# Kernel tuning notes

Measured on AMD Instinct MI355X. Metric: run time of the kernel, lower is better.

Reference implementation:

```python
import jax, jax.numpy as jnp
import numpy as np

BASIS_PRIMES = (2, 3, 5, 7, 11, 13, 17, 19, 23, 29)


def _build_resonance(max_seq):
    # p-adic valuations v_p(n) for n = 1..max_seq, each basis prime (vectorized LUT build)
    n = np.arange(1, max_seq + 1, dtype=np.int64)
    vals = np.zeros((max_seq, len(BASIS_PRIMES)), dtype=np.float32)
    for j, p in enumerate(BASIS_PRIMES):
        m = n.copy()
        while True:
            div = (m % p) == 0
            if not div.any():
                break
            vals[div, j] += 1.0
            m = np.where(div, m // p, m)
    # resonance(a,b) = sum_i min(v_{p_i}(a), v_{p_i}(b))  -> [T, T]
    res = np.zeros((max_seq, max_seq), dtype=np.float32)
    for j in range(len(BASIS_PRIMES)):
        vj = vals[:, j]
        res += np.minimum(vj[:, None], vj[None, :])
    causal = np.tril(np.ones((max_seq, max_seq), dtype=bool))
    allowed = ((res > 0) | np.eye(max_seq, dtype=bool)) & causal
    bias = (np.log1p(res) * allowed).astype(np.float32)
    return bias, allowed


def setup_inputs() -> dict:
    B, T, d_model, head_size, max_seq = 8, 2048, 1024, 128, 2048
    key = jax.random.key(0)
    kx, kq, kk, kv = jax.random.split(key, 4)
    bound = 1.0 / np.sqrt(d_model)  # torch Linear default init range
    x = jax.random.normal(kx, (B, T, d_model), dtype=jnp.float32)
    Wq = jax.random.uniform(kq, (head_size, d_model), jnp.float32, -bound, bound)
    Wk = jax.random.uniform(kk, (head_size, d_model), jnp.float32, -bound, bound)
    Wv = jax.random.uniform(kv, (head_size, d_model), jnp.float32, -bound, bound)
    bias, allowed = _build_resonance(max_seq)
    return {
        "x": x, "Wq": Wq, "Wk": Wk, "Wv": Wv,
        "resonance_bias": jnp.asarray(bias),
        "allowed": jnp.asarray(allowed),
    }


def reference(x, Wq, Wk, Wv, resonance_bias, allowed):
    B, T, C = x.shape
    q = jnp.einsum('btc,hc->bth', x, Wq)
    k = jnp.einsum('btc,hc->bth', x, Wk)
    v = jnp.einsum('btc,hc->bth', x, Wv)
    # NOTE: original scales by C**-0.5 where C = d_model (input channels)
    wei = jnp.einsum('bth,bsh->bts', q, k) * (C ** -0.5)
    wei = wei + resonance_bias[:T, :T]
    neg = jnp.finfo(wei.dtype).min
    wei = jnp.where(allowed[:T, :T], wei, neg)
    wei = jax.nn.softmax(wei, axis=-1)  # dropout is identity in eval mode
    return jnp.einsum('bts,bsh->bth', wei, v)
```

## Files before the change

### kernel.cpp

```cpp
#include <hip/hip_runtime.h>
#include <hip/hip_bf16.h>
#include <stdint.h>

typedef float f32x4  __attribute__((ext_vector_type(4)));
typedef short s16x8  __attribute__((ext_vector_type(8)));
typedef short s16x4  __attribute__((ext_vector_type(4)));
typedef unsigned short u16x8 __attribute__((ext_vector_type(8)));

#define MFMA16(A,B,C) __builtin_amdgcn_mfma_f32_16x16x32_bf16((A),(B),(C),0,0,0)

__device__ __forceinline__ short f2bf(float f) {
    uint32_t u = __float_as_uint(f);
    u += 0x7FFFu + ((u >> 16) & 1u);
    return (short)(u >> 16);
}
__device__ __forceinline__ float bf2f(unsigned short u) {
    return __uint_as_float(((uint32_t)u) << 16);
}
__device__ __forceinline__ int cum_jobs(int qt) {
  int h = qt >> 1;
  return (qt & 1) ? (h + 1) * (h + 1) : h * (h + 1);
}

#define OFF_PB   0u
#define OFF_WPK  8388608u
#define OFF_PQ   9175040u
#define OFF_PK   13369344u
#define OFF_PV   17563648u
#define OFF_PML  21757952u
#define OFF_PO   22863872u
#define WS_SPLIT 60096512u

__global__ __launch_bounds__(256) void pack_misc_kernel(
    const float* __restrict__ wq, const float* __restrict__ wk,
    const float* __restrict__ wv, const float* __restrict__ bias,
    short* __restrict__ Wpk, short* __restrict__ pb) {
  const int tid = threadIdx.x, wid = tid >> 6, lane = tid & 63;
  const int g = lane >> 4, c4 = lane & 15;
  if (blockIdx.x < 192) {
    const int idx = blockIdx.x * 4 + wid;
    const int im = idx >> 8, rest = idx & 255;
    const int ntl = rest >> 5, k32 = rest & 31;
    const float* w = (im == 0) ? wq : (im == 1) ? wk : wv;
    const float* p = w + (size_t)(ntl * 16 + c4) * 1024 + k32 * 32 + 4 * g;
    f32x4 lo = *(const f32x4*)p;
    f32x4 hi = *(const f32x4*)(p + 16);
    s16x8 o = { f2bf(lo[0]), f2bf(lo[1]), f2bf(lo[2]), f2bf(lo[3]),
                f2bf(hi[0]), f2bf(hi[1]), f2bf(hi[2]), f2bf(hi[3]) };
    *(s16x8*)(Wpk + (size_t)idx * 512 + lane * 8) = o;
  } else {
    const int idx = (blockIdx.x - 192) * 4 + wid;
    const int t16 = idx >> 6, s32 = idx & 63;
    const int t = t16 * 16 + c4;
    const int sb = s32 * 32 + 4 * g;
    const float* p = bias + (size_t)t * 2048 + sb;
    f32x4 lo = *(const f32x4*)p;
    f32x4 hi = *(const f32x4*)(p + 16);
    s16x8 o;
    #pragma unroll
    for (int i = 0; i < 4; ++i) {
      int s0 = sb + i, s1 = sb + 16 + i;
      bool ok0 = (s0 <= t) && (s0 == t || lo[i] > 0.f);
      bool ok1 = (s1 <= t) && (s1 == t || hi[i] > 0.f);
      o[i]     = f2bf(ok0 ? lo[i] : -1e30f);
      o[4 + i] = f2bf(ok1 ? hi[i] : -1e30f);
    }
    *(s16x8*)(pb + (size_t)idx * 512 + lane * 8) = o;
  }
}

__global__ __launch_bounds__(256, 2) void qkv_gemm7_kernel(
    const float* __restrict__ x, const short* __restrict__ Wpk,
    short* __restrict__ pq, short* __restrict__ pk, short* __restrict__ pv) {
  const int tid = threadIdx.x, wid = tid >> 6, lane = tid & 63;
  const int g = lane >> 4, c4 = lane & 15;
  const int L8 = lane * 8;
  const int w = blockIdx.x * 4 + wid;
  const int im = w >> 9;
  const int t2 = w & 511;
  const int b = t2 >> 6;
  const float* xrA = x + (size_t)(t2 * 32 + c4) * 1024 + 4 * g;
  const float* xrB = xrA + (size_t)16 * 1024;
  const short* wp = Wpk + (size_t)(im * 256) * 512 + L8;

  f32x4 acc0[8], acc1[8];
  #pragma unroll
  for (int i = 0; i < 8; ++i) {
    acc0[i] = (f32x4){0.f, 0.f, 0.f, 0.f};
    acc1[i] = (f32x4){0.f, 0.f, 0.f, 0.f};
  }

  f32x4 aA0l, aA0h, aA1l, aA1h;
  f32x4 aB0l, aB0h, aB1l, aB1h;
  s16x8 wA[8], wB[8];
#define G7_LDRAW(p0l, p0h, p1l, p1h, kk) { \
    p0l = *(const f32x4*)(xrA + (size_t)(kk) * 32); \
    p0h = *(const f32x4*)(xrA + (size_t)(kk) * 32 + 16); \
    p1l = *(const f32x4*)(xrB + (size_t)(kk) * 32); \
    p1h = *(const f32x4*)(xrB + (size_t)(kk) * 32 + 16); }
#define G7_LDW(dw, kk) { _Pragma("unroll") \
    for (int nt = 0; nt < 8; ++nt) \
      dw[nt] = *(const s16x8*)(wp + (size_t)(nt * 32 + (kk)) * 512); }
#define G7_CVT(fr, lo, hi) \
    s16x8 fr = { f2bf(lo[0]), f2bf(lo[1]), f2bf(lo[2]), f2bf(lo[3]), \
                 f2bf(hi[0]), f2bf(hi[1]), f2bf(hi[2]), f2bf(hi[3]) };

  if (im < 2) {
    G7_LDRAW(aA0l, aA0h, aA1l, aA1h, 0); G7_LDW(wA, 0);
    for (int k = 0; k < 32; k += 2) {
      G7_LDRAW(aB0l, aB0h, aB1l, aB1h, k + 1); G7_LDW(wB, k + 1);
      G7_CVT(xf0, aA0l, aA0h); G7_CVT(xf1, aA1l, aA1h);
      #pragma unroll
      for (int nt = 0; nt < 8; ++nt) {
        acc0[nt] = MFMA16(wA[nt], xf0, acc0[nt]);
        acc1[nt] = MFMA16(wA[nt], xf1, acc1[nt]);
      }
      if (k + 2 < 32) { G7_LDRAW(aA0l, aA0h, aA1l, aA1h, k + 2); G7_LDW(wA, k + 2); }
      G7_CVT(yf0, aB0l, aB0h); G7_CVT(yf1, aB1l, aB1h);
      #pragma unroll
      for (int nt = 0; nt < 8; ++nt) {
        acc0[nt] = MFMA16(wB[nt], yf0, acc0[nt]);
        acc1[nt] = MFMA16(wB[nt], yf1, acc1[nt]);
      }
    }
    short* __restrict__ o = im ? pk : pq;
    const int loc0 = (t2 & 63) * 2;
    #pragma unroll
    for (int f = 0; f < 4; ++f) {
      s16x8 fr0 = { f2bf(acc0[2*f][0]),   f2bf(acc0[2*f][1]),
                    f2bf(acc0[2*f][2]),   f2bf(acc0[2*f][3]),
                    f2bf(acc0[2*f+1][0]), f2bf(acc0[2*f+1][1]),
                    f2bf(acc0[2*f+1][2]), f2bf(acc0[2*f+1][3]) };
      *(s16x8*)(o + (size_t)(b * 512 + loc0 * 4 + f) * 512 + L8) = fr0;
      s16x8 fr1 = { f2bf(acc1[2*f][0]),   f2bf(acc1[2*f][1]),
                    f2bf(acc1[2*f][2]),   f2bf(acc1[2*f][3]),
                    f2bf(acc1[2*f+1][0]), f2bf(acc1[2*f+1][1]),
                    f2bf(acc1[2*f+1][2]), f2bf(acc1[2*f+1][3]) };
      *(s16x8*)(o + (size_t)(b * 512 + (loc0 + 1) * 4 + f) * 512 + L8) = fr1;
    }
  } else {
    G7_LDRAW(aA0l, aA0h, aA1l, aA1h, 0); G7_LDW(wA, 0);
    for (int k = 0; k < 32; k += 2) {
      G7_LDRAW(aB0l, aB0h, aB1l, aB1h, k + 1); G7_LDW(wB, k + 1);
      G7_CVT(xf0, aA0l, aA0h); G7_CVT(xf1, aA1l, aA1h);
      #pragma unroll
      for (int nt = 0; nt < 8; ++nt) {
        acc0[nt] = MFMA16(xf0, wA[nt], acc0[nt]);
        acc1[nt] = MFMA16(xf1, wA[nt], acc1[nt]);
      }
      if (k + 2 < 32) { G7_LDRAW(aA0l, aA0h, aA1l, aA1h, k + 2); G7_LDW(wA, k + 2); }
      G7_CVT(yf0, aB0l, aB0h); G7_CVT(yf1, aB1l, aB1h);
      #pragma unroll
      for (int nt = 0; nt < 8; ++nt) {
        acc0[nt] = MFMA16(yf0, wB[nt], acc0[nt]);
        acc1[nt] = MFMA16(yf1, wB[nt], acc1[nt]);
      }
    }
    const int s32l = t2 & 63;
    #pragma unroll
    for (int nt = 0; nt < 8; ++nt) {
      s16x8 fr = { f2bf(acc0[nt][0]), f2bf(acc0[nt][1]),
                   f2bf(acc0[nt][2]), f2bf(acc0[nt][3]),
                   f2bf(acc1[nt][0]), f2bf(acc1[nt][1]),
                   f2bf(acc1[nt][2]), f2bf(acc1[nt][3]) };
      *(s16x8*)(pv + (size_t)(b * 512 + s32l * 8 + nt) * 512 + L8) = fr;
    }
  }
#undef G7_LDRAW
#undef G7_LDW
#undef G7_CVT
}

template<bool SPLIT>
__global__ __launch_bounds__(128) void attn_kernel(
    const short* __restrict__ pq, const short* __restrict__ pk,
    const short* __restrict__ pv, const short* __restrict__ pb,
    float* __restrict__ out, float* __restrict__ part_ml,
    short* __restrict__ part_o) {
  int qt, c;
  if (SPLIT) {
    const int i = blockIdx.x;
    int h = (int)sqrtf((float)i);
    while (h * h > i) --h;
    while ((h + 1) * (h + 1) <= i) ++h;
    if (i < h * (h + 1)) { qt = 2 * h - 1; c = i - h * h; }
    else                 { qt = 2 * h;     c = i - h * (h + 1); }
  } else {
    qt = blockIdx.x; c = 0;
  }
  const int n = (qt >> 1) + 1;
  const int tid = threadIdx.x;
  const int wid = tid >> 6, lane = tid & 63;
  const int g = lane >> 4, c4 = lane & 15;
  const int b = blockIdx.y;
  const int q16a = qt * 4 + wid * 2;
  const int L8 = lane * 8;

  s16x8 qfa[4], qfb[4];
  #pragma unroll
  for (int f = 0; f < 4; ++f) {
    qfa[f] = *(const s16x8*)(pq + (size_t)(b * 512 + q16a * 4 + f) * 512 + L8);
    qfb[f] = *(const s16x8*)(pq + (size_t)(b * 512 + (q16a + 1) * 4 + f) * 512 + L8);
  }

  float m0 = -1e30f, l0 = 0.f, m1 = -1e30f, l1 = 0.f;
  f32x4 acc0[8], acc1[8];
  #pragma unroll
  for (int i = 0; i < 8; ++i) {
    acc0[i] = (f32x4){0.f, 0.f, 0.f, 0.f};
    acc1[i] = (f32x4){0.f, 0.f, 0.f, 0.f};
  }

  const int q_hi_w = qt * 64 + wid * 32 + 32;
  const int s_begin = SPLIT ? c * 128 : 0;
  const int s_stop  = min(SPLIT ? s_begin + 128 : (1 << 30), q_hi_w);

  for (int s0 = s_begin; s0 < s_stop; s0 += 32) {
    const int s16i = s0 >> 4, s32 = s0 >> 5;
    const short* kbase = pk + (size_t)(b * 512 + s16i * 4) * 512 + L8;
    const short* vbase = pv + (size_t)(b * 512 + s32 * 8) * 512 + L8;
    s16x8 kf0[4], kf1[4];
    #pragma unroll
    for (int f = 0; f < 4; ++f) {
      kf0[f] = *(const s16x8*)(kbase + (size_t)f * 512);
      kf1[f] = *(const s16x8*)(kbase + (size_t)(4 + f) * 512);
    }
    u16x8 bva = *(const u16x8*)(pb + (size_t)(q16a * 64 + s32) * 512 + L8);
    u16x8 bvb = *(const u16x8*)(pb + (size_t)((q16a + 1) * 64 + s32) * 512 + L8);
    f32x4 s0a = (f32x4){0.f,0.f,0.f,0.f}, s1a = (f32x4){0.f,0.f,0.f,0.f};
    f32x4 s0b = (f32x4){0.f,0.f,0.f,0.f}, s1b = (f32x4){0.f,0.f,0.f,0.f};
    __builtin_amdgcn_s_setprio(1);
    #pragma unroll
    for (int f = 0; f < 4; ++f) {
      s0a = MFMA16(kf0[f], qfa[f], s0a);
      s1a = MFMA16(kf1[f], qfa[f], s1a);
      s0b = MFMA16(kf0[f], qfb[f], s0b);
      s1b = MFMA16(kf1[f], qfb[f], s1b);
    }
    __builtin_amdgcn_s_setprio(0);
    float va[8], vb[8];
    #pragma unroll
    for (int st = 0; st < 2; ++st)
      #pragma unroll
      for (int r = 0; r < 4; ++r) {
        va[st * 4 + r] = (st ? s1a[r] : s0a[r]) * 0.03125f + bf2f(bva[st * 4 + r]);
        vb[st * 4 + r] = (st ? s1b[r] : s0b[r]) * 0.03125f + bf2f(bvb[st * 4 + r]);
      }
    float mva = va[0], mvb = vb[0];
    #pragma unroll
    for (int i = 1; i < 8; ++i) { mva = fmaxf(mva, va[i]); mvb = fmaxf(mvb, vb[i]); }
    mva = fmaxf(mva, __shfl_xor(mva, 16)); mva = fmaxf(mva, __shfl_xor(mva, 32));
    mvb = fmaxf(mvb, __shfl_xor(mvb, 16)); mvb = fmaxf(mvb, __shfl_xor(mvb, 32));
    if (!__all((mva <= m0 + 8.f) && (mvb <= m1 + 8.f))) {
      float mn0 = fmaxf(m0, mva), mn1 = fmaxf(m1, mvb);
      float a0 = __expf(m0 - mn0), a1 = __expf(m1 - mn1);
      l0 *= a0; l1 *= a1; m0 = mn0; m1 = mn1;
      float ar0[4], ar1[4];
      #pragma unroll
      for (int r = 0; r < 4; ++r) {
        ar0[r] = __shfl(a0, (lane & 48) | (4 * g + r));
        ar1[r] = __shfl(a1, (lane & 48) | (4 * g + r));
      }
      #pragma unroll
      for (int nt = 0; nt < 8; ++nt)
        #pragma unroll
        for (int r = 0; r < 4; ++r) {
          acc0[nt][r] *= ar0[r];
          acc1[nt][r] *= ar1[r];
        }
    }
    float pa8[8], pb8[8], psa = 0.f, psb = 0.f;
    #pragma unroll
    for (int i = 0; i < 8; ++i) {
      pa8[i] = (va[i] > -1e29f) ? __expf(va[i] - m0) : 0.f;  psa += pa8[i];
      pb8[i] = (vb[i] > -1e29f) ? __expf(vb[i] - m1) : 0.f;  psb += pb8[i];
    }
    psa += __shfl_xor(psa, 16); psa += __shfl_xor(psa, 32); l0 += psa;
    psb += __shfl_xor(psb, 16); psb += __shfl_xor(psb, 32); l1 += psb;
    s16x8 paf = { f2bf(pa8[0]), f2bf(pa8[1]), f2bf(pa8[2]), f2bf(pa8[3]),
                  f2bf(pa8[4]), f2bf(pa8[5]), f2bf(pa8[6]), f2bf(pa8[7]) };
    s16x8 pbf = { f2bf(pb8[0]), f2bf(pb8[1]), f2bf(pb8[2]), f2bf(pb8[3]),
                  f2bf(pb8[4]), f2bf(pb8[5]), f2bf(pb8[6]), f2bf(pb8[7]) };
    __builtin_amdgcn_s_setprio(1);
    #pragma unroll
    for (int nt = 0; nt < 8; ++nt) {
      s16x8 vf = *(const s16x8*)(vbase + (size_t)nt * 512);
      acc0[nt] = MFMA16(paf, vf, acc0[nt]);
      acc1[nt] = MFMA16(pbf, vf, acc1[nt]);
    }
    __builtin_amdgcn_s_setprio(0);
  }

  if (!SPLIT || n == 1) {
    float li0 = 1.f / l0, li1 = 1.f / l1;
    float lr0[4], lr1[4];
    #pragma unroll
    for (int r = 0; r < 4; ++r) {
      lr0[r] = __shfl(li0, (lane & 48) | (4 * g + r));
      lr1[r] = __shfl(li1, (lane & 48) | (4 * g + r));
    }
    const int row0 = qt * 64 + wid * 32;
    #pragma unroll
    for (int nt = 0; nt < 8; ++nt)
      #pragma unroll
      for (int r = 0; r < 4; ++r) {
        out[(size_t)(b * 2048 + row0 + 4 * g + r) * 128 + 16 * nt + c4] =
            acc0[nt][r] * lr0[r];
        out[(size_t)(b * 2048 + row0 + 16 + 4 * g + r) * 128 + 16 * nt + c4] =
            acc1[nt][r] * lr1[r];
      }
  } else {
    const int slot = b * 270 + cum_jobs(qt) - 2 + c;
    short* po = part_o + (size_t)slot * 8192 + (size_t)(wid * 8) * 512 + L8;
    #pragma unroll
    for (int nt = 0; nt < 8; ++nt) {
      s16x8 fr = { f2bf(acc0[nt][0]), f2bf(acc0[nt][1]),
                   f2bf(acc0[nt][2]), f2bf(acc0[nt][3]),
                   f2bf(acc1[nt][0]), f2bf(acc1[nt][1]),
                   f2bf(acc1[nt][2]), f2bf(acc1[nt][3]) };
      *(s16x8*)(po + (size_t)nt * 512) = fr;
    }
    if (lane < 16) {
      part_ml[slot * 128 + wid * 32 + c4]           = m0;
      part_ml[slot * 128 + wid * 32 + 16 + c4]      = m1;
      part_ml[slot * 128 + 64 + wid * 32 + c4]      = l0;
      part_ml[slot * 128 + 64 + wid * 32 + 16 + c4] = l1;
    }
  }
}

__global__ __launch_bounds__(256) void combine_kernel(
    const float* __restrict__ part_ml, const unsigned short* __restrict__ part_o,
    float* __restrict__ out) {
  const int qt = 2 + blockIdx.x;
  const int b = blockIdx.y;
  const int n = (qt >> 1) + 1;
  const int slot0 = b * 270 + cum_jobs(qt) - 2;
  const int tid = threadIdx.x;

  __shared__ float scl[16][64];
  if (tid < 64) {
    const int r = tid;
    float M = -1e30f;
    for (int cc = 0; cc < n; ++cc)
      M = fmaxf(M, part_ml[(size_t)(slot0 + cc) * 128 + r]);
    float L = 0.f;
    for (int cc = 0; cc < n; ++cc)
      L += part_ml[(size_t)(slot0 + cc) * 128 + 64 + r] *
           __expf(part_ml[(size_t)(slot0 + cc) * 128 + r] - M);
    float inv = 1.f / L;
    for (int cc = 0; cc < n; ++cc)
      scl[cc][r] = __expf(part_ml[(size_t)(slot0 + cc) * 128 + r] - M) * inv;
  }
  __syncthreads();
  const int fgr = tid >> 6, lane = tid & 63;
  const int g = lane >> 4, c4 = lane & 15;
  for (int ff = fgr; ff < 16; ff += 4) {
    const int rbase = (ff >> 3) * 32 + 4 * g;
    const int col = (ff & 7) * 16 + c4;
    float o[8] = {0.f,0.f,0.f,0.f,0.f,0.f,0.f,0.f};
    for (int cc = 0; cc < n; ++cc) {
      u16x8 v = *(const u16x8*)(part_o +
          (size_t)(slot0 + cc) * 8192 + (size_t)ff * 512 + lane * 8);
      #pragma unroll
      for (int j = 0; j < 8; ++j)
        o[j] += bf2f(v[j]) * scl[cc][rbase + (j >> 2) * 16 + (j & 3)];
    }
    #pragma unroll
    for (int j = 0; j < 8; ++j) {
      const int row = rbase + (j >> 2) * 16 + (j & 3);
      out[(size_t)(b * 2048 + qt * 64 + row) * 128 + col] = o[j];
    }
  }
}

extern "C" void kernel_launch(void* const* d_in, const int* in_sizes, int n_in,
                              void* d_out, int out_size, void* d_ws, size_t ws_size,
                              hipStream_t stream) {
  const float* x    = (const float*)d_in[0];
  const float* wq   = (const float*)d_in[1];
  const float* wk   = (const float*)d_in[2];
  const float* wv   = (const float*)d_in[3];
  const float* bias = (const float*)d_in[4];

  char* ws = (char*)d_ws;
  short* pb      = (short*)(ws + OFF_PB);
  short* Wpk     = (short*)(ws + OFF_WPK);
  short* pq      = (short*)(ws + OFF_PQ);
  short* pk      = (short*)(ws + OFF_PK);
  short* pv      = (short*)(ws + OFF_PV);
  float* part_ml = (float*)(ws + OFF_PML);
  short* part_o  = (short*)(ws + OFF_PO);
  float* outp    = (float*)d_out;

  pack_misc_kernel<<<2240, 256, 0, stream>>>(wq, wk, wv, bias, Wpk, pb);
  qkv_gemm7_kernel<<<384, 256, 0, stream>>>(x, Wpk, pq, pk, pv);

  if (ws_size >= WS_SPLIT) {
    attn_kernel<true><<<dim3(272, 8), 128, 0, stream>>>(
        pq, pk, pv, pb, outp, part_ml, part_o);
    combine_kernel<<<dim3(30, 8), 256, 0, stream>>>(
        part_ml, (const unsigned short*)part_o, outp);
  } else {
    attn_kernel<false><<<dim3(32, 8), 128, 0, stream>>>(
        pq, pk, pv, pb, outp, part_ml, part_o);
  }
}
```

Baseline: 109.2 us.

## Share x tile across Q/K/V waves via double-buffered LDS in QKV GEMM

The QKV projection now gives each block one 32-row x tile. Its threads convert x to bf16 once and stage it into a double-buffered LDS tile, which all four waves read. Waves 0 and 1 compute Q and K, and waves 2 and 3 each compute half of V. Before, each wave streamed and converted its own fp32 x rows, so x was read three times from global memory. The change removes that redundant traffic and conversion at the cost of a __syncthreads per K step and a drop from two-deep register prefetch to one-deep.

```diff
diff --git a/kernel.cpp b/kernel.cpp
--- a/kernel.cpp
+++ b/kernel.cpp
@@ -69,61 +69,56 @@
   }
 }
 
-__global__ __launch_bounds__(256, 2) void qkv_gemm7_kernel(
+__global__ __launch_bounds__(256, 2) void qkv_gemm8_kernel(
     const float* __restrict__ x, const short* __restrict__ Wpk,
     short* __restrict__ pq, short* __restrict__ pk, short* __restrict__ pv) {
+  __shared__ short lx[2][1024];
   const int tid = threadIdx.x, wid = tid >> 6, lane = tid & 63;
   const int g = lane >> 4, c4 = lane & 15;
   const int L8 = lane * 8;
-  const int w = blockIdx.x * 4 + wid;
-  const int im = w >> 9;
-  const int t2 = w & 511;
+  const int t2 = blockIdx.x;
   const int b = t2 >> 6;
-  const float* xrA = x + (size_t)(t2 * 32 + c4) * 1024 + 4 * g;
-  const float* xrB = xrA + (size_t)16 * 1024;
-  const short* wp = Wpk + (size_t)(im * 256) * 512 + L8;
-
-  f32x4 acc0[8], acc1[8];
-  #pragma unroll
-  for (int i = 0; i < 8; ++i) {
-    acc0[i] = (f32x4){0.f, 0.f, 0.f, 0.f};
-    acc1[i] = (f32x4){0.f, 0.f, 0.f, 0.f};
-  }
-
-  f32x4 aA0l, aA0h, aA1l, aA1h;
-  f32x4 aB0l, aB0h, aB1l, aB1h;
-  s16x8 wA[8], wB[8];
-#define G7_LDRAW(p0l, p0h, p1l, p1h, kk) { \
-    p0l = *(const f32x4*)(xrA + (size_t)(kk) * 32); \
-    p0h = *(const f32x4*)(xrA + (size_t)(kk) * 32 + 16); \
-    p1l = *(const f32x4*)(xrB + (size_t)(kk) * 32); \
-    p1h = *(const f32x4*)(xrB + (size_t)(kk) * 32 + 16); }
-#define G7_LDW(dw, kk) { _Pragma("unroll") \
-    for (int nt = 0; nt < 8; ++nt) \
-      dw[nt] = *(const s16x8*)(wp + (size_t)(nt * 32 + (kk)) * 512); }
-#define G7_CVT(fr, lo, hi) \
-    s16x8 fr = { f2bf(lo[0]), f2bf(lo[1]), f2bf(lo[2]), f2bf(lo[3]), \
-                 f2bf(hi[0]), f2bf(hi[1]), f2bf(hi[2]), f2bf(hi[3]) };
-
-  if (im < 2) {
-    G7_LDRAW(aA0l, aA0h, aA1l, aA1h, 0); G7_LDW(wA, 0);
-    for (int k = 0; k < 32; k += 2) {
-      G7_LDRAW(aB0l, aB0h, aB1l, aB1h, k + 1); G7_LDW(wB, k + 1);
-      G7_CVT(xf0, aA0l, aA0h); G7_CVT(xf1, aA1l, aA1h);
+  const int srow = tid >> 3, scg = tid & 7;
+  const float* xs = x + (size_t)(t2 * 32 + srow) * 1024 + scg * 4;
+  const int swoff = (srow >> 4) * 512 + (((scg & 3) * 16 + (srow & 15)) * 8)
+                  + (scg >> 2) * 4;
+  {
+    f32x4 xv = *(const f32x4*)xs;
+    s16x4 sv = { f2bf(xv[0]), f2bf(xv[1]), f2bf(xv[2]), f2bf(xv[3]) };
+    *(s16x4*)&lx[0][swoff] = sv;
+  }
+  __syncthreads();
+
+  if (wid < 2) {
+    const short* wp = Wpk + (size_t)(wid * 256) * 512 + L8;
+    f32x4 acc0[8], acc1[8];
+    #pragma unroll
+    for (int i = 0; i < 8; ++i) {
+      acc0[i] = (f32x4){0.f, 0.f, 0.f, 0.f};
+      acc1[i] = (f32x4){0.f, 0.f, 0.f, 0.f};
+    }
+    for (int k = 0; k < 32; ++k) {
+      f32x4 xn;
+      if (k < 31) xn = *(const f32x4*)(xs + (size_t)(k + 1) * 32);
+      s16x8 wf[8];
+      #pragma unroll
+      for (int nt = 0; nt < 8; ++nt)
+        wf[nt] = *(const s16x8*)(wp + (size_t)(nt * 32 + k) * 512);
+      const short* lb = &lx[k & 1][0];
+      s16x8 xf0 = *(const s16x8*)(lb + L8);
+      s16x8 xf1 = *(const s16x8*)(lb + 512 + L8);
       #pragma unroll
       for (int nt = 0; nt < 8; ++nt) {
-        acc0[nt] = MFMA16(wA[nt], xf0, acc0[nt]);
-        acc1[nt] = MFMA16(wA[nt], xf1, acc1[nt]);
-      }
-      if (k + 2 < 32) { G7_LDRAW(aA0l, aA0h, aA1l, aA1h, k + 2); G7_LDW(wA, k + 2); }
-      G7_CVT(yf0, aB0l, aB0h); G7_CVT(yf1, aB1l, aB1h);
-      #pragma unroll
-      for (int nt = 0; nt < 8; ++nt) {
-        acc0[nt] = MFMA16(wB[nt], yf0, acc0[nt]);
-        acc1[nt] = MFMA16(wB[nt], yf1, acc1[nt]);
-      }
-    }
-    short* __restrict__ o = im ? pk : pq;
+        acc0[nt] = MFMA16(wf[nt], xf0, acc0[nt]);
+        acc1[nt] = MFMA16(wf[nt], xf1, acc1[nt]);
+      }
+      if (k < 31) {
+        s16x4 sv = { f2bf(xn[0]), f2bf(xn[1]), f2bf(xn[2]), f2bf(xn[3]) };
+        *(s16x4*)&lx[(k + 1) & 1][swoff] = sv;
+      }
+      __syncthreads();
+    }
+    short* __restrict__ o = wid ? pk : pq;
     const int loc0 = (t2 & 63) * 2;
     #pragma unroll
     for (int f = 0; f < 4; ++f) {
@@ -139,36 +134,45 @@
       *(s16x8*)(o + (size_t)(b * 512 + (loc0 + 1) * 4 + f) * 512 + L8) = fr1;
     }
   } else {
-    G7_LDRAW(aA0l, aA0h, aA1l, aA1h, 0); G7_LDW(wA, 0);
-    for (int k = 0; k < 32; k += 2) {
-      G7_LDRAW(aB0l, aB0h, aB1l, aB1h, k + 1); G7_LDW(wB, k + 1);
-      G7_CVT(xf0, aA0l, aA0h); G7_CVT(xf1, aA1l, aA1h);
-      #pragma unroll
-      for (int nt = 0; nt < 8; ++nt) {
-        acc0[nt] = MFMA16(xf0, wA[nt], acc0[nt]);
-        acc1[nt] = MFMA16(xf1, wA[nt], acc1[nt]);
-      }
-      if (k + 2 < 32) { G7_LDRAW(aA0l, aA0h, aA1l, aA1h, k + 2); G7_LDW(wA, k + 2); }
-      G7_CVT(yf0, aB0l, aB0h); G7_CVT(yf1, aB1l, aB1h);
-      #pragma unroll
-      for (int nt = 0; nt < 8; ++nt) {
-        acc0[nt] = MFMA16(yf0, wB[nt], acc0[nt]);
-        acc1[nt] = MFMA16(yf1, wB[nt], acc1[nt]);
-      }
+    const int ntoff = (wid - 2) * 4;
+    const short* wp = Wpk + (size_t)(512 + ntoff * 32) * 512 + L8;
+    f32x4 acc0[4], acc1[4];
+    #pragma unroll
+    for (int i = 0; i < 4; ++i) {
+      acc0[i] = (f32x4){0.f, 0.f, 0.f, 0.f};
+      acc1[i] = (f32x4){0.f, 0.f, 0.f, 0.f};
+    }
+    for (int k = 0; k < 32; ++k) {
+      f32x4 xn;
+      if (k < 31) xn = *(const f32x4*)(xs + (size_t)(k + 1) * 32);
+      s16x8 wf[4];
+      #pragma unroll
+      for (int j = 0; j < 4; ++j)
+        wf[j] = *(const s16x8*)(wp + (size_t)(j * 32 + k) * 512);
+      const short* lb = &lx[k & 1][0];
+      s16x8 xf0 = *(const s16x8*)(lb + L8);
+      s16x8 xf1 = *(const s16x8*)(lb + 512 + L8);
+      #pragma unroll
+      for (int j = 0; j < 4; ++j) {
+        acc0[j] = MFMA16(xf0, wf[j], acc0[j]);
+        acc1[j] = MFMA16(xf1, wf[j], acc1[j]);
+      }
+      if (k < 31) {
+        s16x4 sv = { f2bf(xn[0]), f2bf(xn[1]), f2bf(xn[2]), f2bf(xn[3]) };
+        *(s16x4*)&lx[(k + 1) & 1][swoff] = sv;
+      }
+      __syncthreads();
     }
     const int s32l = t2 & 63;
     #pragma unroll
-    for (int nt = 0; nt < 8; ++nt) {
-      s16x8 fr = { f2bf(acc0[nt][0]), f2bf(acc0[nt][1]),
-                   f2bf(acc0[nt][2]), f2bf(acc0[nt][3]),
-                   f2bf(acc1[nt][0]), f2bf(acc1[nt][1]),
-                   f2bf(acc1[nt][2]), f2bf(acc1[nt][3]) };
-      *(s16x8*)(pv + (size_t)(b * 512 + s32l * 8 + nt) * 512 + L8) = fr;
-    }
-  }
-#undef G7_LDRAW
-#undef G7_LDW
-#undef G7_CVT
+    for (int j = 0; j < 4; ++j) {
+      s16x8 fr = { f2bf(acc0[j][0]), f2bf(acc0[j][1]),
+                   f2bf(acc0[j][2]), f2bf(acc0[j][3]),
+                   f2bf(acc1[j][0]), f2bf(acc1[j][1]),
+                   f2bf(acc1[j][2]), f2bf(acc1[j][3]) };
+      *(s16x8*)(pv + (size_t)(b * 512 + s32l * 8 + ntoff + j) * 512 + L8) = fr;
+    }
+  }
 }
 
 template<bool SPLIT>
@@ -394,7 +398,7 @@
   float* outp    = (float*)d_out;
 
   pack_misc_kernel<<<2240, 256, 0, stream>>>(wq, wk, wv, bias, Wpk, pb);
-  qkv_gemm7_kernel<<<384, 256, 0, stream>>>(x, Wpk, pq, pk, pv);
+  qkv_gemm8_kernel<<<512, 256, 0, stream>>>(x, Wpk, pq, pk, pv);
 
   if (ws_size >= WS_SPLIT) {
     attn_kernel<true><<<dim3(272, 8), 128, 0, stream>>>(
```

After: 104.1 us. 1.05x faster.
